# Optimization experiments

Measured on AMD Instinct MI355X. Metric: run time of the kernel, lower is better.

The kernel has to match this reference:

```python
import jax, jax.numpy as jnp
import numpy as np


def _rx(state, theta, axis):
    # Apply RX(theta) to qubit at tensor axis `axis`. state: (B, 2,...,2) complex.
    half = theta * 0.5
    c = jnp.cos(half)
    s = jnp.sin(half)
    a0 = jnp.take(state, 0, axis=axis)
    a1 = jnp.take(state, 1, axis=axis)
    return jnp.stack([c * a0 - 1j * s * a1, c * a1 - 1j * s * a0], axis=axis)


def _cnot(state, w):
    # CNOT with control wire w (axis w+1), target wire w+1 (axis w+2).
    c_ax = w + 1
    s0 = jnp.take(state, 0, axis=c_ax)
    # after removing the control axis, the target axis index becomes c_ax
    s1 = jnp.flip(jnp.take(state, 1, axis=c_ax), axis=c_ax)
    return jnp.stack([s0, s1], axis=c_ax)


def _run_circuit(x, params):
    # x: (B, n) encoding angles; params: (depth, n) trainable RX angles.
    B, n = x.shape
    depth = params.shape[0]
    state = jnp.zeros((B,) + (2,) * n, jnp.complex64)
    state = state.at[(slice(None),) + (0,) * n].set(1.0 + 0.0j)
    # angle encoding: RX(x_w) on each wire
    for w in range(n):
        theta = x[:, w].reshape((B,) + (1,) * (n - 1))
        state = _rx(state, theta, w + 1)
    # variational layers: RX(param) per wire, then CNOT chain
    for d in range(depth):
        for w in range(n):
            state = _rx(state, params[d, w], w + 1)
        for w in range(n - 1):
            state = _cnot(state, w)
    probs = state.real ** 2 + state.imag ** 2  # (B, 2,...,2)
    ez = []
    for w in range(n):
        axes = tuple(a for a in range(1, n + 1) if a != w + 1)
        p = probs.sum(axes)  # (B, 2)
        ez.append(p[:, 0] - p[:, 1])  # <Z_w>
    return jnp.stack(ez, axis=1)  # (B, n)


def setup_inputs() -> dict:
    key = jax.random.key(0)
    k0, k1, k2, k3, k4 = jax.random.split(key, 5)
    seq_len, batch, input_dim = 256, 128, 64
    n_qubits, depth, hidden = 10, 2, 256
    inputs = jax.random.normal(k0, (seq_len, batch, input_dim), jnp.float32)
    mask = jax.random.randint(k1, (seq_len, batch), 0, 2).astype(jnp.int32)
    qparams = jax.random.normal(k2, (4, depth, n_qubits), jnp.float32)
    W = jax.random.normal(k3, (4, hidden, n_qubits), jnp.float32) / np.sqrt(n_qubits)
    b = jax.random.normal(k4, (4, hidden), jnp.float32) * 0.01
    return {"inputs": inputs, "mask": mask, "qparams": qparams, "W": W, "b": b}


def reference(inputs, mask, qparams, W, b):
    seq_len, batch, _ = inputs.shape
    n = qparams.shape[-1]
    hidden = W.shape[1]
    maskf = mask.astype(inputs.dtype)

    circuits4 = jax.vmap(_run_circuit, in_axes=(None, 0))  # over the 4 gates

    def step(carry, xm):
        hx, cx = carry
        x_t, m_t = xm
        q_in = jnp.concatenate([x_t, hx], axis=1)[:, :n]  # (B, n)
        z = circuits4(q_in, qparams)                      # (4, B, n)
        pre = jnp.einsum('gbn,ghn->gbh', z, W) + b[:, None, :]
        f = jax.nn.sigmoid(pre[0])
        i = jax.nn.sigmoid(pre[1])
        g = jnp.tanh(pre[2])
        o = jax.nn.sigmoid(pre[3])
        m = m_t[:, None]
        f = f * m + (1.0 - m)
        i = i * m
        g = g * m
        o = o * m + (1.0 - m)
        cx_new = f * cx + i * g
        hx_new = o * jnp.tanh(cx_new)
        return (hx_new, cx_new), hx_new

    h0 = jnp.zeros((batch, hidden), inputs.dtype)
    c0 = jnp.zeros((batch, hidden), inputs.dtype)
    (hx, cx), outputs = jax.lax.scan(jax.checkpoint(step), (h0, c0), (inputs, maskf))
    return outputs, (hx, cx)
```

## Files before the change

kernel.cpp:

```cpp
#include <hip/hip_runtime.h>

#define T_LEN 256
#define BATCH 128
#define NQ 10
#define NG 4
#define HID 256
#define OUT_HX (T_LEN * BATCH * HID)
#define OUT_CX (OUT_HX + BATCH * HID)

__global__ __launch_bounds__(512) void qlstm_kernel(
    const float* __restrict__ inputs,
    const int*  __restrict__ mask,
    const float* __restrict__ qparams,
    const float* __restrict__ W,
    const float* __restrict__ bias,
    float* __restrict__ out)
{
  const int b    = blockIdx.x;
  const int half = blockIdx.y;
  const int tid  = threadIdx.x;
  const int g    = tid & 3;
  const int ch   = tid >> 2;
  const int h    = half * 128 + ch;

  __shared__ __align__(16) float zs[T_LEN][48];
  __shared__ float mk[T_LEN];
  __shared__ float th0_s[NG * NQ], cth_s[NG * NQ], sth_s[NG * NQ];

  if (tid < NG * NQ) {
    int gg = tid / NQ, k = tid - gg * NQ;
    th0_s[tid] = qparams[gg * 2 * NQ + k];
    float t1   = qparams[gg * 2 * NQ + NQ + k];
    sth_s[tid] = __sinf(t1);
    cth_s[tid] = __cosf(t1);
  }
  for (int t = tid; t < T_LEN; t += 512) mk[t] = (float)mask[t * BATCH + b];
  __syncthreads();

  for (int inst = tid; inst < T_LEN * NG; inst += 512) {
    int t = inst >> 2, gg = inst & 3;
    float cphi[NQ], sphi[NQ];
#pragma unroll
    for (int k = 0; k < NQ; ++k) {
      float ang = inputs[(t * BATCH + b) * 64 + k] + th0_s[gg * NQ + k];
      sphi[k] = __sinf(ang);
      cphi[k] = __cosf(ang);
    }
    const float* cth = cth_s + gg * NQ;
    const float* sth = sth_s + gg * NQ;
#pragma unroll
    for (int w = 0; w < NQ; ++w) {
      float vI, vZ, vY, vX; int js;
      if (w == NQ - 1) { vI = 0.f; vZ = cth[NQ-1]; vY = sth[NQ-1]; vX = 0.f; js = NQ - 2; }
      else             { vI = 1.f; vZ = 0.f; vY = 0.f; vX = 0.f; js = w; }
#pragma unroll
      for (int j = js; j >= 0; --j) {
        float nI = cth[j] * (cphi[j+1] * vZ - sphi[j+1] * vY);
        float nZ = cth[j] * vI;
        float nY = sth[j] * vX;
        float nX = -sth[j] * (sphi[j+1] * vZ + cphi[j+1] * vY);
        vI = nI; vZ = nZ; vY = nY; vX = nX;
      }
      zs[t][gg * 12 + w] = vI + cphi[0] * vZ - sphi[0] * vY;
    }
  }
  __syncthreads();

  float Wreg[NQ];
#pragma unroll
  for (int n = 0; n < NQ; ++n) Wreg[n] = W[(g * HID + h) * NQ + n];
  float bg = bias[g * HID + h];

  const float scale_in = (g == 2) ? -2.f : -1.f;
  const float a_c  = (g == 2) ? 2.f : 1.f;
  const float bt_c = (g == 2) ? -1.f : 0.f;
  const float d_c  = (g == 0 || g == 3) ? 1.f : 0.f;

  const int g12 = g * 12;
  float4 za = *(const float4*)&zs[0][g12];
  float4 zb = *(const float4*)&zs[0][g12 + 4];
  float2 zc = *(const float2*)&zs[0][g12 + 8];
  float mcur = mk[0];

  float c = 0.f, hv = 0.f;
  float* outp = out + b * HID + h;

  for (int t = 0; t < T_LEN; ++t) {
    int tn = (t + 1 < T_LEN) ? t + 1 : t;
    float4 na = *(const float4*)&zs[tn][g12];
    float4 nb = *(const float4*)&zs[tn][g12 + 4];
    float2 nc = *(const float2*)&zs[tn][g12 + 8];
    float mnext = mk[tn];

    float acc0 = fmaf(za.x, Wreg[0], bg);
    acc0 = fmaf(za.y, Wreg[1], acc0);
    acc0 = fmaf(za.z, Wreg[2], acc0);
    acc0 = fmaf(za.w, Wreg[3], acc0);
    acc0 = fmaf(zc.x, Wreg[8], acc0);
    float acc1 = zb.x * Wreg[4];
    acc1 = fmaf(zb.y, Wreg[5], acc1);
    acc1 = fmaf(zb.z, Wreg[6], acc1);
    acc1 = fmaf(zb.w, Wreg[7], acc1);
    acc1 = fmaf(zc.y, Wreg[9], acc1);
    float pre = acc0 + acc1;

    float e = __expf(scale_in * pre);
    float u = __builtin_amdgcn_rcpf(1.f + e);
    float val = fmaf(mcur, fmaf(a_c, u, bt_c), d_c * (1.f - mcur));

    float v1 = __shfl_xor(val, 1, 64);
    float v2 = __shfl_xor(val, 2, 64);
    float v3 = __shfl_xor(v1, 2, 64);

    if (g == 0) {
      c = fmaf(val, c, v1 * v2);
      float e2 = __expf(-2.f * c);
      float tc = fmaf(2.f, __builtin_amdgcn_rcpf(1.f + e2), -1.f);
      hv = v3 * tc;
      outp[t * (BATCH * HID)] = hv;
    }
    za = na; zb = nb; zc = nc; mcur = mnext;
  }
  if (g == 0) {
    out[OUT_HX + b * HID + h] = hv;
    out[OUT_CX + b * HID + h] = c;
  }
}

extern "C" void kernel_launch(void* const* d_in, const int* in_sizes, int n_in,
                              void* d_out, int out_size, void* d_ws, size_t ws_size,
                              hipStream_t stream)
{
  int ii = 0, im = 1, iq = 2, iw = 3, ib = 4;
  for (int i = 0; i < n_in; ++i) {
    switch (in_sizes[i]) {
      case 2097152: ii = i; break;
      case 32768:   im = i; break;
      case 80:      iq = i; break;
      case 10240:   iw = i; break;
      case 1024:    ib = i; break;
      default: break;
    }
  }
  const float* inputs  = (const float*)d_in[ii];
  const int*   mask    = (const int*)d_in[im];
  const float* qparams = (const float*)d_in[iq];
  const float* W       = (const float*)d_in[iw];
  const float* bias    = (const float*)d_in[ib];
  float*       out     = (float*)d_out;

  qlstm_kernel<<<dim3(BATCH, 2), dim3(512), 0, stream>>>(
      inputs, mask, qparams, W, bias, out);
}
```

Before: 120.8 us.

## Split quantum-expectation precompute into separate kernel and chunk the LSTM scan

The per-timestep circuit expectation values are now computed by a standalone, fully parallel kernel into a workspace buffer, instead of redundantly inside each scan block. The scan kernel uses 4 hidden-quarters per batch row (512 blocks of 256 threads), streams z in 64-step chunks, and only runs the cell-state recurrence serially. Output gate and tanh(c) are deferred to a parallel post-pass per chunk that writes h with coalesced stores. This adds a global-memory round trip for z and extra syncs/shared buffers.

Measured after the change: 130.6 us. +8.1%, slower.

```diff
diff --git a/kernel.cpp b/kernel.cpp
--- a/kernel.cpp
+++ b/kernel.cpp
@@ -3,128 +3,138 @@
 #define T_LEN 256
 #define BATCH 128
 #define NQ 10
-#define NG 4
 #define HID 256
 #define OUT_HX (T_LEN * BATCH * HID)
 #define OUT_CX (OUT_HX + BATCH * HID)
+#define ZSTRIDE 48
+#define TC 64
+#define NCH 64
 
-__global__ __launch_bounds__(512) void qlstm_kernel(
-    const float* __restrict__ inputs,
-    const int*  __restrict__ mask,
-    const float* __restrict__ qparams,
-    const float* __restrict__ W,
-    const float* __restrict__ bias,
+__global__ __launch_bounds__(256) void zcalc_kernel(
+    const float* __restrict__ x, const float* __restrict__ qp,
+    float* __restrict__ zg)
+{
+  const int flat = blockIdx.x * 256 + threadIdx.x;
+  const int g = flat & 3, tb = flat >> 2;
+  const int t = tb >> 7, b = tb & 127;
+
+  float cphi[NQ], sphi[NQ], cth[NQ], sth[NQ];
+#pragma unroll
+  for (int k = 0; k < NQ; ++k) {
+    float ang = x[tb * 64 + k] + qp[g * 20 + k];
+    sphi[k] = __sinf(ang);  cphi[k] = __cosf(ang);
+    float t1 = qp[g * 20 + 10 + k];
+    sth[k] = __sinf(t1);    cth[k] = __cosf(t1);
+  }
+  float* zp = zg + (b * T_LEN + t) * ZSTRIDE + g * 12;
+#pragma unroll
+  for (int w = 0; w < NQ; ++w) {
+    float vI, vZ, vY, vX; int js;
+    if (w == NQ - 1) { vI = 0.f; vZ = cth[NQ-1]; vY = sth[NQ-1]; vX = 0.f; js = NQ - 2; }
+    else             { vI = 1.f; vZ = 0.f; vY = 0.f; vX = 0.f; js = w; }
+#pragma unroll
+    for (int j = js; j >= 0; --j) {
+      float nI = cth[j] * (cphi[j+1] * vZ - sphi[j+1] * vY);
+      float nZ = cth[j] * vI;
+      float nY = sth[j] * vX;
+      float nX = -sth[j] * (sphi[j+1] * vZ + cphi[j+1] * vY);
+      vI = nI; vZ = nZ; vY = nY; vX = nX;
+    }
+    zp[w] = vI + cphi[0] * vZ - sphi[0] * vY;
+  }
+}
+
+__global__ __launch_bounds__(256) void scan_kernel(
+    const float* __restrict__ zg, const int* __restrict__ mask,
+    const float* __restrict__ W, const float* __restrict__ bias,
     float* __restrict__ out)
 {
-  const int b    = blockIdx.x;
-  const int half = blockIdx.y;
-  const int tid  = threadIdx.x;
-  const int g    = tid & 3;
-  const int ch   = tid >> 2;
-  const int h    = half * 128 + ch;
+  const int b   = blockIdx.x;
+  const int hq  = blockIdx.y;
+  const int tid = threadIdx.x;
+  const int g   = tid & 3;
+  const int ch  = tid >> 2;
+  const int h   = hq * 64 + ch;
 
-  __shared__ __align__(16) float zs[T_LEN][48];
+  __shared__ __align__(16) float zs[TC][ZSTRIDE];
+  __shared__ float cbuf[TC][NCH + 1];
+  __shared__ float p3buf[TC][NCH + 1];
   __shared__ float mk[T_LEN];
-  __shared__ float th0_s[NG * NQ], cth_s[NG * NQ], sth_s[NG * NQ];
-
-  if (tid < NG * NQ) {
-    int gg = tid / NQ, k = tid - gg * NQ;
-    th0_s[tid] = qparams[gg * 2 * NQ + k];
-    float t1   = qparams[gg * 2 * NQ + NQ + k];
-    sth_s[tid] = __sinf(t1);
-    cth_s[tid] = __cosf(t1);
-  }
-  for (int t = tid; t < T_LEN; t += 512) mk[t] = (float)mask[t * BATCH + b];
-  __syncthreads();
-
-  for (int inst = tid; inst < T_LEN * NG; inst += 512) {
-    int t = inst >> 2, gg = inst & 3;
-    float cphi[NQ], sphi[NQ];
-#pragma unroll
-    for (int k = 0; k < NQ; ++k) {
-      float ang = inputs[(t * BATCH + b) * 64 + k] + th0_s[gg * NQ + k];
-      sphi[k] = __sinf(ang);
-      cphi[k] = __cosf(ang);
-    }
-    const float* cth = cth_s + gg * NQ;
-    const float* sth = sth_s + gg * NQ;
-#pragma unroll
-    for (int w = 0; w < NQ; ++w) {
-      float vI, vZ, vY, vX; int js;
-      if (w == NQ - 1) { vI = 0.f; vZ = cth[NQ-1]; vY = sth[NQ-1]; vX = 0.f; js = NQ - 2; }
-      else             { vI = 1.f; vZ = 0.f; vY = 0.f; vX = 0.f; js = w; }
-#pragma unroll
-      for (int j = js; j >= 0; --j) {
-        float nI = cth[j] * (cphi[j+1] * vZ - sphi[j+1] * vY);
-        float nZ = cth[j] * vI;
-        float nY = sth[j] * vX;
-        float nX = -sth[j] * (sphi[j+1] * vZ + cphi[j+1] * vY);
-        vI = nI; vZ = nZ; vY = nY; vX = nX;
-      }
-      zs[t][gg * 12 + w] = vI + cphi[0] * vZ - sphi[0] * vY;
-    }
-  }
-  __syncthreads();
 
   float Wreg[NQ];
 #pragma unroll
   for (int n = 0; n < NQ; ++n) Wreg[n] = W[(g * HID + h) * NQ + n];
-  float bg = bias[g * HID + h];
+  const float bg = bias[g * HID + h];
+
+  for (int t0 = tid; t0 < T_LEN; t0 += 256) mk[t0] = (float)mask[t0 * BATCH + b];
 
   const float scale_in = (g == 2) ? -2.f : -1.f;
   const float a_c  = (g == 2) ? 2.f : 1.f;
   const float bt_c = (g == 2) ? -1.f : 0.f;
-  const float d_c  = (g == 0 || g == 3) ? 1.f : 0.f;
+  const float d_c  = (g == 0) ? 1.f : 0.f;
 
+  float c = 0.f;
+  const float4* zsrc = (const float4*)(zg + b * T_LEN * ZSTRIDE);
   const int g12 = g * 12;
-  float4 za = *(const float4*)&zs[0][g12];
-  float4 zb = *(const float4*)&zs[0][g12 + 4];
-  float2 zc = *(const float2*)&zs[0][g12 + 8];
-  float mcur = mk[0];
 
-  float c = 0.f, hv = 0.f;
-  float* outp = out + b * HID + h;
+  for (int ck = 0; ck < T_LEN / TC; ++ck) {
+    const int tt = ck * TC;
+    {
+      float4* dst = (float4*)&zs[0][0];
+#pragma unroll
+      for (int i = 0; i < 3; ++i)
+        dst[i * 256 + tid] = zsrc[tt * (ZSTRIDE / 4) + i * 256 + tid];
+    }
+    __syncthreads();
 
-  for (int t = 0; t < T_LEN; ++t) {
-    int tn = (t + 1 < T_LEN) ? t + 1 : t;
-    float4 na = *(const float4*)&zs[tn][g12];
-    float4 nb = *(const float4*)&zs[tn][g12 + 4];
-    float2 nc = *(const float2*)&zs[tn][g12 + 8];
-    float mnext = mk[tn];
+#pragma unroll 8
+    for (int s = 0; s < TC; ++s) {
+      float4 za = *(const float4*)&zs[s][g12];
+      float4 zb = *(const float4*)&zs[s][g12 + 4];
+      float2 zc = *(const float2*)&zs[s][g12 + 8];
+      float acc0 = fmaf(za.x, Wreg[0], bg);
+      acc0 = fmaf(za.y, Wreg[1], acc0);
+      acc0 = fmaf(za.z, Wreg[2], acc0);
+      acc0 = fmaf(za.w, Wreg[3], acc0);
+      acc0 = fmaf(zc.x, Wreg[8], acc0);
+      float acc1 = zb.x * Wreg[4];
+      acc1 = fmaf(zb.y, Wreg[5], acc1);
+      acc1 = fmaf(zb.z, Wreg[6], acc1);
+      acc1 = fmaf(zb.w, Wreg[7], acc1);
+      acc1 = fmaf(zc.y, Wreg[9], acc1);
+      float pre = acc0 + acc1;
+      if (g == 3) p3buf[s][ch] = pre;
+      float m = mk[tt + s];
+      float e = __expf(scale_in * pre);
+      float u = __builtin_amdgcn_rcpf(1.f + e);
+      float val = fmaf(m, fmaf(a_c, u, bt_c), d_c * (1.f - m));
+      float v1 = __shfl_xor(val, 1, 64);
+      float v2 = __shfl_xor(val, 2, 64);
+      if (g == 0) {
+        c = fmaf(val, c, v1 * v2);
+        cbuf[s][ch] = c;
+      }
+    }
+    __syncthreads();
 
-    float acc0 = fmaf(za.x, Wreg[0], bg);
-    acc0 = fmaf(za.y, Wreg[1], acc0);
-    acc0 = fmaf(za.z, Wreg[2], acc0);
-    acc0 = fmaf(za.w, Wreg[3], acc0);
-    acc0 = fmaf(zc.x, Wreg[8], acc0);
-    float acc1 = zb.x * Wreg[4];
-    acc1 = fmaf(zb.y, Wreg[5], acc1);
-    acc1 = fmaf(zb.z, Wreg[6], acc1);
-    acc1 = fmaf(zb.w, Wreg[7], acc1);
-    acc1 = fmaf(zc.y, Wreg[9], acc1);
-    float pre = acc0 + acc1;
-
-    float e = __expf(scale_in * pre);
-    float u = __builtin_amdgcn_rcpf(1.f + e);
-    float val = fmaf(mcur, fmaf(a_c, u, bt_c), d_c * (1.f - mcur));
-
-    float v1 = __shfl_xor(val, 1, 64);
-    float v2 = __shfl_xor(val, 2, 64);
-    float v3 = __shfl_xor(v1, 2, 64);
-
-    if (g == 0) {
-      c = fmaf(val, c, v1 * v2);
-      float e2 = __expf(-2.f * c);
-      float tc = fmaf(2.f, __builtin_amdgcn_rcpf(1.f + e2), -1.f);
-      hv = v3 * tc;
-      outp[t * (BATCH * HID)] = hv;
+#pragma unroll
+    for (int i = 0; i < 16; ++i) {
+      int p = i * 256 + tid;
+      int lt = p >> 6, lch = p & 63;
+      int t = tt + lt;
+      float cv = cbuf[lt][lch];
+      float p3 = p3buf[lt][lch];
+      float m = mk[t];
+      float eo = __expf(-p3);
+      float o  = fmaf(m, __builtin_amdgcn_rcpf(1.f + eo), 1.f - m);
+      float e2 = __expf(-2.f * cv);
+      float tc2 = fmaf(2.f, __builtin_amdgcn_rcpf(1.f + e2), -1.f);
+      float hv = o * tc2;
+      out[t * (BATCH * HID) + b * HID + hq * 64 + lch] = hv;
+      if (t == T_LEN - 1) out[OUT_HX + b * HID + hq * 64 + lch] = hv;
     }
-    za = na; zb = nb; zc = nc; mcur = mnext;
   }
-  if (g == 0) {
-    out[OUT_HX + b * HID + h] = hv;
-    out[OUT_CX + b * HID + h] = c;
-  }
+  if (g == 0) out[OUT_CX + b * HID + h] = c;
 }
 
 extern "C" void kernel_launch(void* const* d_in, const int* in_sizes, int n_in,
@@ -149,6 +159,10 @@
   const float* bias    = (const float*)d_in[ib];
   float*       out     = (float*)d_out;
 
-  qlstm_kernel<<<dim3(BATCH, 2), dim3(512), 0, stream>>>(
-      inputs, mask, qparams, W, bias, out);
+  float* zg = (float*)d_ws;
+
+  zcalc_kernel<<<dim3(T_LEN * BATCH * 4 / 256), dim3(256), 0, stream>>>(
+      inputs, qparams, zg);
+  scan_kernel<<<dim3(BATCH, 4), dim3(256), 0, stream>>>(
+      zg, mask, W, bias, out);
 }
```
